# Kernel tuning notes

Hardware: AMD Instinct MI355X
Metric: run time of the kernel (lower is better)

Reference implementation:

```python
import jax, jax.numpy as jnp
import numpy as np

NEG_BIG = -9e15
ALPHA = 0.2  # leaky relu slope


def setup_inputs() -> dict:
    key = jax.random.key(0)
    k1, k2, k3, k4 = jax.random.split(key, 4)
    B, N, Fin, Fout = 8, 2048, 128, 64
    h = jax.random.normal(k1, (B, N, Fin), dtype=jnp.float32)
    adj = jax.random.randint(k2, (B, N, N), 0, 2, dtype=jnp.int32)
    # xavier_uniform-like init scale
    W = jax.random.uniform(k3, (Fin, Fout), dtype=jnp.float32, minval=-1.0, maxval=1.0) * (1.414 * np.sqrt(6.0 / (Fin + Fout)))
    a = jax.random.uniform(k4, (2 * Fout, 1), dtype=jnp.float32, minval=-1.0, maxval=1.0) * (1.414 * np.sqrt(6.0 / (2 * Fout + 1)))
    return {"h": h, "adj": adj, "W": W, "a": a}


def reference(h, adj, W, a):
    # h: [B,N,Fin], adj: [B,N,N], W: [Fin,Fout], a: [2*Fout,1]
    Fout = W.shape[1]
    Wh = jnp.einsum('bni,io->bno', h, W)            # [B,N,Fout]
    # e_ij = leakyrelu(a[:Fout] . Wh_i + a[Fout:] . Wh_j)  (decomposed, same math
    # as the original concat + matmul with a)
    f_src = Wh @ a[:Fout, 0]                        # [B,N]
    f_dst = Wh @ a[Fout:, 0]                        # [B,N]
    e = f_src[:, :, None] + f_dst[:, None, :]       # [B,N,N]
    e = jnp.where(e > 0, e, ALPHA * e)              # leaky relu
    e = jnp.where(adj > 0, e, NEG_BIG)              # mask
    attention = jax.nn.softmax(e, axis=2)           # [B,N,N]
    h_prime = jnp.einsum('bnm,bmo->bno', attention, Wh)
    return jax.nn.elu(h_prime)
```

## Files before the change

### kernel.cpp

```cpp
#include <hip/hip_runtime.h>
#include <hip/hip_bf16.h>

constexpr int Bb  = 8;
constexpr int Nn  = 2048;
constexpr int FIN = 128;
constexpr int FOUT = 64;
constexpr float LOG2E = 1.4426950408889634f;

typedef __bf16 bf16x8 __attribute__((ext_vector_type(8)));
typedef __bf16 bf16x2 __attribute__((ext_vector_type(2)));
typedef float  f32x4  __attribute__((ext_vector_type(4)));
typedef int    i32x4  __attribute__((ext_vector_type(4)));
typedef unsigned int u32;

__device__ __forceinline__ u32 f2bf_bits(float f) {
    u32 u = __builtin_bit_cast(u32, f);
    return (u + 0x7FFFu + ((u >> 16) & 1u)) >> 16;
}

__global__ __launch_bounds__(256) void gat_k1(
        const float* __restrict__ h, const float* __restrict__ W,
        const float* __restrict__ a, __bf16* __restrict__ whfrag,
        float* __restrict__ fs, float* __restrict__ fd) {
    const int blk = blockIdx.x;
    const int b   = blk >> 6;
    const int t32 = blk & 63;
    const int n0  = t32 * 32;
    const int l   = threadIdx.x & 63;
    const int w   = __builtin_amdgcn_readfirstlane((int)(threadIdx.x >> 6));

    __shared__ __align__(16) float hT[32][FIN];

    {
        const float4* hb = reinterpret_cast<const float4*>(h + (size_t)(b * Nn + n0) * FIN);
        float4* dst = reinterpret_cast<float4*>(&hT[0][0]);
#pragma unroll
        for (int k = 0; k < 4; ++k) {
            const int flat = threadIdx.x + k * 256;
            dst[flat] = hb[flat];
        }
    }
    __syncthreads();

    const float a0 = a[l];
    const float a1 = a[FOUT + l];

    float acc[8];
#pragma unroll
    for (int r = 0; r < 8; ++r) acc[r] = 0.f;

#pragma unroll 1
    for (int c0 = 0; c0 < FIN; c0 += 32) {
        float wreg[32];
#pragma unroll
        for (int cc = 0; cc < 32; ++cc) wreg[cc] = W[(c0 + cc) * FOUT + l];
#pragma unroll
        for (int r = 0; r < 8; ++r) {
            const int row = w * 8 + r;
#pragma unroll
            for (int cc = 0; cc < 32; ++cc)
                acc[r] = fmaf(hT[row][c0 + cc], wreg[cc], acc[r]);
        }
    }

#pragma unroll
    for (int r = 0; r < 8; ++r) {
        float s0 = acc[r] * a0;
        float s1 = acc[r] * a1;
#pragma unroll
        for (int off = 32; off >= 1; off >>= 1) {
            s0 += __shfl_xor(s0, off, 64);
            s1 += __shfl_xor(s1, off, 64);
        }
        if (l == 0) {
            fs[b * Nn + n0 + w * 8 + r] = s0 * LOG2E;
            fd[b * Nn + n0 + w * 8 + r] = s1 * LOG2E;
        }
    }

    u32 pk[4];
#pragma unroll
    for (int i = 0; i < 4; ++i)
        pk[i] = f2bf_bits(acc[2 * i]) | (f2bf_bits(acc[2 * i + 1]) << 16);
    const int slotg = ((b * 64 + t32) * 4 + (l >> 4)) * 64 + ((w << 4) | (l & 15));
    reinterpret_cast<uint4*>(whfrag)[slotg] = make_uint4(pk[0], pk[1], pk[2], pk[3]);
}

__global__ __launch_bounds__(256, 3) void gat_k2(
        const int* __restrict__ adj, const __bf16* __restrict__ whfrag,
        const float* __restrict__ fs, const float* __restrict__ fd,
        float* __restrict__ out) {
    const int blk = blockIdx.x;
    const int b   = blk >> 7;
    const int i0  = (blk & 127) * 16;
    const int l   = threadIdx.x & 63;
    const int w   = __builtin_amdgcn_readfirstlane((int)(threadIdx.x >> 6));

    __shared__ __align__(16) char  aLDS[4 * 8192];
    __shared__ f32x4 comb[4][4][64];
    __shared__ float zpart[4][16];

    const int hi = l >> 5;
    const int lo = l & 31;
    const int g  = l >> 4;
    const int jc = l & 15;

    char* myA = aLDS + w * 8192;

    float fs_loc[8];
#pragma unroll
    for (int t = 0; t < 8; ++t) fs_loc[t] = fs[b * Nn + i0 + 2 * t + hi];

    const int    jq0  = w * 512;
    const float* fdp  = fd + b * Nn + jq0 + lo * 4;
    const int*   adj0 = adj + (size_t)(b * Nn + i0 + hi) * Nn + jq0 + lo * 4;

    const bf16x8* bfr = reinterpret_cast<const bf16x8*>(whfrag)
                        + (size_t)(b * 256) * 64 + l;

    f32x4 acc[4] = {{0,0,0,0},{0,0,0,0},{0,0,0,0},{0,0,0,0}};
    f32x4 accz   = {0.f, 0.f, 0.f, 0.f};

    bf16x8 onesv;
#pragma unroll
    for (int i = 0; i < 8; ++i) onesv[i] = (__bf16)1.0f;

    i32x4 adjT[2][8];
    f32x4 fdQ[2];

#pragma unroll
    for (int t = 0; t < 8; ++t)
        adjT[0][t] = *reinterpret_cast<const i32x4*>(adj0 + (size_t)(2 * t) * Nn);
    fdQ[0] = *reinterpret_cast<const f32x4*>(fdp);

#pragma unroll 2
    for (int it = 0; it < 4; ++it) {
        const int cur = it & 1, nxt = cur ^ 1;
        if (it < 3) {
#pragma unroll
            for (int t = 0; t < 8; ++t)
                adjT[nxt][t] = *reinterpret_cast<const i32x4*>(
                                   adj0 + (size_t)(2 * t) * Nn + (it + 1) * 128);
            fdQ[nxt] = *reinterpret_cast<const f32x4*>(fdp + (it + 1) * 128);
        }

        char* buf = myA + cur * 4096;
#pragma unroll
        for (int t = 0; t < 8; ++t) {
            const int row = 2 * t + hi;
            float pv[4];
#pragma unroll
            for (int q = 0; q < 4; ++q) {
                float e  = fs_loc[t] + fdQ[cur][q];
                float lr = fmaxf(e, 0.2f * e);
                float p  = exp2f(lr);
                pv[q] = (adjT[cur][t][q] > 0) ? p : 0.f;
            }
            u32 w0 = __builtin_bit_cast(u32, (bf16x2){(__bf16)pv[0], (__bf16)pv[1]});
            u32 w1 = __builtin_bit_cast(u32, (bf16x2){(__bf16)pv[2], (__bf16)pv[3]});
            const int boff = (row * 256 + lo * 8) ^ ((row & 7) << 4);
            *reinterpret_cast<uint2*>(buf + boff) = make_uint2(w0, w1);
        }

        asm volatile("s_waitcnt lgkmcnt(0)" ::: "memory");
        __builtin_amdgcn_sched_barrier(0x20);

#pragma unroll
        for (int kb = 0; kb < 4; ++kb) {
            const int rbyte = (((l & 15) * 256 + kb * 64 + (l >> 4) * 16)
                               ^ ((l & 7) << 4));
            bf16x8 av = *reinterpret_cast<const bf16x8*>(buf + rbyte);
            const int t32 = w * 16 + it * 4 + kb;
#pragma unroll
            for (int o16 = 0; o16 < 4; ++o16)
                acc[o16] = __builtin_amdgcn_mfma_f32_16x16x32_bf16(
                               av, bfr[(t32 * 4 + o16) * 64], acc[o16], 0, 0, 0);
            accz = __builtin_amdgcn_mfma_f32_16x16x32_bf16(av, onesv, accz, 0, 0, 0);
        }
    }

    if ((l & 15) == 0) {
#pragma unroll
        for (int r = 0; r < 4; ++r) zpart[w][(l >> 4) * 4 + r] = accz[r];
    }
#pragma unroll
    for (int o16 = 0; o16 < 4; ++o16) comb[w][o16][l] = acc[o16];
    __syncthreads();

    f32x4 res = comb[0][w][l];
#pragma unroll
    for (int wp = 1; wp < 4; ++wp) res += comb[wp][w][l];

#pragma unroll
    for (int r = 0; r < 4; ++r) {
        const int row = g * 4 + r;
        float z = zpart[0][row] + zpart[1][row] + zpart[2][row] + zpart[3][row];
        float v = res[r] / z;
        v = v > 0.f ? v : expm1f(v);
        out[(size_t)(b * Nn + i0 + row) * FOUT + w * 16 + jc] = v;
    }
}

extern "C" void kernel_launch(void* const* d_in, const int* in_sizes, int n_in,
                              void* d_out, int out_size, void* d_ws, size_t ws_size,
                              hipStream_t stream) {
    const float* h   = (const float*)d_in[0];
    const int*   adj = (const int*)d_in[1];
    const float* W   = (const float*)d_in[2];
    const float* a   = (const float*)d_in[3];
    float* out = (float*)d_out;

    __bf16* whfrag = (__bf16*)d_ws;
    float*  fs     = (float*)((char*)d_ws + (size_t)Bb * Nn * FOUT * 2);
    float*  fd     = fs + Bb * Nn;

    gat_k1<<<dim3(Bb * 64), dim3(256), 0, stream>>>(h, W, a, whfrag, fs, fd);
    gat_k2<<<dim3(Bb * 128), dim3(256), 0, stream>>>(adj, whfrag, fs, fd, out);
}
```

Before: 55.59 us.

## Restructure GAT attention loop into 64-column steps with triple-buffered prefetch

The per-wave attention loop now processes 64 columns per step instead of 128, with each lane handling four consecutive rows. Adjacency and f_dst loads are prefetched two steps ahead through a three-slot register ring, in a fully unrolled macro. Per-wave LDS shrinks to half and launch bounds rise to 4 blocks per CU, aiming for more occupancy and deeper latency hiding on the adjacency stream. The trade-off is more LDS wait/sync points per column and possible register pressure under the tighter occupancy bound.

```diff
diff --git a/kernel.cpp b/kernel.cpp
--- a/kernel.cpp
+++ b/kernel.cpp
@@ -86,7 +86,7 @@
     reinterpret_cast<uint4*>(whfrag)[slotg] = make_uint4(pk[0], pk[1], pk[2], pk[3]);
 }
 
-__global__ __launch_bounds__(256, 3) void gat_k2(
+__global__ __launch_bounds__(256, 4) void gat_k2(
         const int* __restrict__ adj, const __bf16* __restrict__ whfrag,
         const float* __restrict__ fs, const float* __restrict__ fd,
         float* __restrict__ out) {
@@ -96,27 +96,25 @@
     const int l   = threadIdx.x & 63;
     const int w   = __builtin_amdgcn_readfirstlane((int)(threadIdx.x >> 6));
 
-    __shared__ __align__(16) char  aLDS[4 * 8192];
+    __shared__ __align__(16) char  aLDS[4 * 4096];
     __shared__ f32x4 comb[4][4][64];
     __shared__ float zpart[4][16];
 
-    const int hi = l >> 5;
-    const int lo = l & 31;
     const int g  = l >> 4;
     const int jc = l & 15;
 
-    char* myA = aLDS + w * 8192;
-
-    float fs_loc[8];
-#pragma unroll
-    for (int t = 0; t < 8; ++t) fs_loc[t] = fs[b * Nn + i0 + 2 * t + hi];
+    char* myA = aLDS + w * 4096;
+
+    float fs_loc[4];
+#pragma unroll
+    for (int rr = 0; rr < 4; ++rr) fs_loc[rr] = fs[b * Nn + i0 + g * 4 + rr];
 
     const int    jq0  = w * 512;
-    const float* fdp  = fd + b * Nn + jq0 + lo * 4;
-    const int*   adj0 = adj + (size_t)(b * Nn + i0 + hi) * Nn + jq0 + lo * 4;
+    const float* fdp  = fd + b * Nn + jq0 + jc * 4;
+    const int*   adj0 = adj + (size_t)(b * Nn + i0 + g * 4) * Nn + jq0 + jc * 4;
 
     const bf16x8* bfr = reinterpret_cast<const bf16x8*>(whfrag)
-                        + (size_t)(b * 256) * 64 + l;
+                        + (size_t)((b * 64 + w * 16) * 4) * 64 + l;
 
     f32x4 acc[4] = {{0,0,0,0},{0,0,0,0},{0,0,0,0},{0,0,0,0}};
     f32x4 accz   = {0.f, 0.f, 0.f, 0.f};
@@ -125,59 +123,79 @@
 #pragma unroll
     for (int i = 0; i < 8; ++i) onesv[i] = (__bf16)1.0f;
 
-    i32x4 adjT[2][8];
-    f32x4 fdQ[2];
-
-#pragma unroll
-    for (int t = 0; t < 8; ++t)
-        adjT[0][t] = *reinterpret_cast<const i32x4*>(adj0 + (size_t)(2 * t) * Nn);
-    fdQ[0] = *reinterpret_cast<const f32x4*>(fdp);
-
-#pragma unroll 2
-    for (int it = 0; it < 4; ++it) {
-        const int cur = it & 1, nxt = cur ^ 1;
-        if (it < 3) {
-#pragma unroll
-            for (int t = 0; t < 8; ++t)
-                adjT[nxt][t] = *reinterpret_cast<const i32x4*>(
-                                   adj0 + (size_t)(2 * t) * Nn + (it + 1) * 128);
-            fdQ[nxt] = *reinterpret_cast<const f32x4*>(fdp + (it + 1) * 128);
-        }
-
-        char* buf = myA + cur * 4096;
-#pragma unroll
-        for (int t = 0; t < 8; ++t) {
-            const int row = 2 * t + hi;
-            float pv[4];
-#pragma unroll
-            for (int q = 0; q < 4; ++q) {
-                float e  = fs_loc[t] + fdQ[cur][q];
-                float lr = fmaxf(e, 0.2f * e);
-                float p  = exp2f(lr);
-                pv[q] = (adjT[cur][t][q] > 0) ? p : 0.f;
-            }
-            u32 w0 = __builtin_bit_cast(u32, (bf16x2){(__bf16)pv[0], (__bf16)pv[1]});
-            u32 w1 = __builtin_bit_cast(u32, (bf16x2){(__bf16)pv[2], (__bf16)pv[3]});
-            const int boff = (row * 256 + lo * 8) ^ ((row & 7) << 4);
-            *reinterpret_cast<uint2*>(buf + boff) = make_uint2(w0, w1);
-        }
-
-        asm volatile("s_waitcnt lgkmcnt(0)" ::: "memory");
-        __builtin_amdgcn_sched_barrier(0x20);
-
-#pragma unroll
-        for (int kb = 0; kb < 4; ++kb) {
-            const int rbyte = (((l & 15) * 256 + kb * 64 + (l >> 4) * 16)
-                               ^ ((l & 7) << 4));
-            bf16x8 av = *reinterpret_cast<const bf16x8*>(buf + rbyte);
-            const int t32 = w * 16 + it * 4 + kb;
-#pragma unroll
-            for (int o16 = 0; o16 < 4; ++o16)
-                acc[o16] = __builtin_amdgcn_mfma_f32_16x16x32_bf16(
-                               av, bfr[(t32 * 4 + o16) * 64], acc[o16], 0, 0, 0);
-            accz = __builtin_amdgcn_mfma_f32_16x16x32_bf16(av, onesv, accz, 0, 0, 0);
-        }
-    }
+    i32x4 adjR[3][4];
+    f32x4 fdR[3];
+
+#pragma unroll
+    for (int rr = 0; rr < 4; ++rr) {
+        adjR[0][rr] = *reinterpret_cast<const i32x4*>(adj0 + (size_t)rr * Nn);
+        adjR[1][rr] = *reinterpret_cast<const i32x4*>(adj0 + (size_t)rr * Nn + 64);
+    }
+    fdR[0] = *reinterpret_cast<const f32x4*>(fdp);
+    fdR[1] = *reinterpret_cast<const f32x4*>(fdp + 64);
+
+#define GAT_STEP(IT, CUR, PRE)                                                 \
+  {                                                                            \
+    if ((IT) + 2 < 8) {                \
+      _Pragma("unroll")                                                        \
+      for (int rr = 0; rr < 4; ++rr)                                           \
+        adjR[PRE][rr] = *reinterpret_cast<const i32x4*>(                       \
+            adj0 + (size_t)rr * Nn + ((IT) + 2) * 64);                         \
+      fdR[PRE] = *reinterpret_cast<const f32x4*>(fdp + ((IT) + 2) * 64);       \
+    }                                                                          \
+    char* buf = myA + ((IT) & 1) * 2048;                                       \
+    _Pragma("unroll")                                                          \
+    for (int rr = 0; rr < 4; ++rr) {                                           \
+      const int row = g * 4 + rr;                                              \
+      u32 wds[2];                                                              \
+      _Pragma("unroll")                                                        \
+      for (int hp = 0; hp < 2; ++hp) {                                         \
+        float pv[2];                                                           \
+        _Pragma("unroll")                                                      \
+        for (int q = 0; q < 2; ++q) {                                          \
+          const int jj = hp * 2 + q;                                           \
+          float e  = fs_loc[rr] + fdR[CUR][jj];                                \
+          float lr = fmaxf(e, 0.2f * e);          \
+          float p  = exp2f(lr);                 \
+          pv[q] = (adjR[CUR][rr][jj] > 0) ? p : 0.f;                           \
+        }                                                                      \
+        wds[hp] = __builtin_bit_cast(u32,                                      \
+                      (bf16x2){(__bf16)pv[0], (__bf16)pv[1]});                 \
+      }                                                                        \
+      const int boff = (row * 128 + jc * 8) ^ ((row & 7) << 4);                \
+      *reinterpret_cast<uint2*>(buf + boff) = make_uint2(wds[0], wds[1]);      \
+    }                                                                          \
+    asm volatile("s_waitcnt lgkmcnt(0)" ::: "memory");                         \
+    __builtin_amdgcn_sched_barrier(0x20);            \
+    {                                                                          \
+      const int rb0 = (((l & 15) * 128 + g * 16) ^ ((l & 7) << 4));            \
+      bf16x8 av = *reinterpret_cast<const bf16x8*>(buf + rb0);                 \
+      _Pragma("unroll")                                                        \
+      for (int o16 = 0; o16 < 4; ++o16)                                        \
+        acc[o16] = __builtin_amdgcn_mfma_f32_16x16x32_bf16(                    \
+            av, bfr[(((IT) * 2 + 0) * 4 + o16) * 64], acc[o16], 0, 0, 0);      \
+      accz = __builtin_amdgcn_mfma_f32_16x16x32_bf16(av, onesv, accz, 0, 0, 0);\
+    }                                                                          \
+    {                                                                          \
+      const int rb1 = (((l & 15) * 128 + 64 + g * 16) ^ ((l & 7) << 4));       \
+      bf16x8 av = *reinterpret_cast<const bf16x8*>(buf + rb1);                 \
+      _Pragma("unroll")                                                        \
+      for (int o16 = 0; o16 < 4; ++o16)                                        \
+        acc[o16] = __builtin_amdgcn_mfma_f32_16x16x32_bf16(                    \
+            av, bfr[(((IT) * 2 + 1) * 4 + o16) * 64], acc[o16], 0, 0, 0);      \
+      accz = __builtin_amdgcn_mfma_f32_16x16x32_bf16(av, onesv, accz, 0, 0, 0);\
+    }                                                                          \
+  }
+
+    GAT_STEP(0, 0, 2)
+    GAT_STEP(1, 1, 0)
+    GAT_STEP(2, 2, 1)
+    GAT_STEP(3, 0, 2)
+    GAT_STEP(4, 1, 0)
+    GAT_STEP(5, 2, 1)
+    GAT_STEP(6, 0, 2)
+    GAT_STEP(7, 1, 0)
+#undef GAT_STEP
 
     if ((l & 15) == 0) {
 #pragma unroll
```

Measured after the change: 47.58 us. 14.4% less time.

## Precompress adjacency into bitmask and build attention MFMA operands in registers

Applied to the files above, without the earlier changes.

The first kernel gains extra blocks that read the int32 adjacency matrix and pack it into a 1-bit-per-entry mask, running alongside the Wh projection blocks. The attention kernel then reads the small mask instead of the full adjacency matrix. It builds the bf16 probability fragments directly in registers in MFMA layout, which removes the LDS staging round-trip and its waits. Total adjacency traffic is unchanged but moves into a streaming pack kernel, and the mask adds an extra workspace write and read.

```diff
diff --git a/kernel.cpp b/kernel.cpp
--- a/kernel.cpp
+++ b/kernel.cpp
@@ -12,24 +12,51 @@
 typedef float  f32x4  __attribute__((ext_vector_type(4)));
 typedef int    i32x4  __attribute__((ext_vector_type(4)));
 typedef unsigned int u32;
+typedef unsigned long long u64;
 
 __device__ __forceinline__ u32 f2bf_bits(float f) {
     u32 u = __builtin_bit_cast(u32, f);
     return (u + 0x7FFFu + ((u >> 16) & 1u)) >> 16;
 }
 
-__global__ __launch_bounds__(256) void gat_k1(
-        const float* __restrict__ h, const float* __restrict__ W,
-        const float* __restrict__ a, __bf16* __restrict__ whfrag,
-        float* __restrict__ fs, float* __restrict__ fd) {
+__global__ __launch_bounds__(256) void gat_k01(
+        const float* __restrict__ h, const int* __restrict__ adj,
+        const float* __restrict__ W, const float* __restrict__ a,
+        __bf16* __restrict__ whfrag, float* __restrict__ fs,
+        float* __restrict__ fd, u64* __restrict__ mask) {
+    __shared__ __align__(16) float hT[32][FIN];
+
+    const int l = threadIdx.x & 63;
+    const int w = __builtin_amdgcn_readfirstlane((int)(threadIdx.x >> 6));
+
+    if (blockIdx.x >= 512) {
+        const size_t gw = (size_t)(blockIdx.x - 512) * 4 + w;
+        const int* p  = adj + gw * 4096 + 4 * l;
+        u64* mout     = mask + gw * 64;
+        i32x4 vv[2];
+        vv[0] = *reinterpret_cast<const i32x4*>(p);
+#pragma unroll
+        for (int i = 0; i < 16; ++i) {
+            const int cur = i & 1;
+            if (i < 15)
+                vv[cur ^ 1] = *reinterpret_cast<const i32x4*>(p + (i + 1) * 256);
+            const i32x4 v = vv[cur];
+            u32 nib = (v[0] > 0 ? 1u : 0u) | (v[1] > 0 ? 2u : 0u) |
+                      (v[2] > 0 ? 4u : 0u) | (v[3] > 0 ? 8u : 0u);
+            u32 x = nib | (((u32)__shfl_xor((int)nib, 1)) << 4);
+            x |= ((u32)__shfl_xor((int)x, 2)) << 8;
+            x |= ((u32)__shfl_xor((int)x, 4)) << 16;
+            u32 hi = (u32)__shfl_xor((int)x, 8);
+            if ((l & 15) == 0)
+                mout[i * 4 + (l >> 4)] = (u64)x | ((u64)hi << 32);
+        }
+        return;
+    }
+
     const int blk = blockIdx.x;
     const int b   = blk >> 6;
     const int t32 = blk & 63;
     const int n0  = t32 * 32;
-    const int l   = threadIdx.x & 63;
-    const int w   = __builtin_amdgcn_readfirstlane((int)(threadIdx.x >> 6));
-
-    __shared__ __align__(16) float hT[32][FIN];
 
     {
         const float4* hb = reinterpret_cast<const float4*>(h + (size_t)(b * Nn + n0) * FIN);
@@ -86,8 +113,8 @@
     reinterpret_cast<uint4*>(whfrag)[slotg] = make_uint4(pk[0], pk[1], pk[2], pk[3]);
 }
 
-__global__ __launch_bounds__(256, 3) void gat_k2(
-        const int* __restrict__ adj, const __bf16* __restrict__ whfrag,
+__global__ __launch_bounds__(256, 4) void gat_k2(
+        const u64* __restrict__ mask, const __bf16* __restrict__ whfrag,
         const float* __restrict__ fs, const float* __restrict__ fd,
         float* __restrict__ out) {
     const int blk = blockIdx.x;
@@ -96,27 +123,19 @@
     const int l   = threadIdx.x & 63;
     const int w   = __builtin_amdgcn_readfirstlane((int)(threadIdx.x >> 6));
 
-    __shared__ __align__(16) char  aLDS[4 * 8192];
     __shared__ f32x4 comb[4][4][64];
     __shared__ float zpart[4][16];
 
-    const int hi = l >> 5;
-    const int lo = l & 31;
-    const int g  = l >> 4;
-    const int jc = l & 15;
-
-    char* myA = aLDS + w * 8192;
-
-    float fs_loc[8];
-#pragma unroll
-    for (int t = 0; t < 8; ++t) fs_loc[t] = fs[b * Nn + i0 + 2 * t + hi];
-
-    const int    jq0  = w * 512;
-    const float* fdp  = fd + b * Nn + jq0 + lo * 4;
-    const int*   adj0 = adj + (size_t)(b * Nn + i0 + hi) * Nn + jq0 + lo * 4;
+    const int row16 = l & 15;
+    const int seg8  = (l >> 4) * 8;
+
+    const float fsr = fs[b * Nn + i0 + row16];
+
+    const u64*   mrow = mask + ((size_t)b * Nn + i0 + row16) * 32 + w * 8;
+    const float* fdq  = fd + b * Nn + w * 512 + seg8;
 
     const bf16x8* bfr = reinterpret_cast<const bf16x8*>(whfrag)
-                        + (size_t)(b * 256) * 64 + l;
+                        + (size_t)((b * 64 + w * 16) * 4) * 64 + l;
 
     f32x4 acc[4] = {{0,0,0,0},{0,0,0,0},{0,0,0,0},{0,0,0,0}};
     f32x4 accz   = {0.f, 0.f, 0.f, 0.f};
@@ -125,56 +144,42 @@
 #pragma unroll
     for (int i = 0; i < 8; ++i) onesv[i] = (__bf16)1.0f;
 
-    i32x4 adjT[2][8];
-    f32x4 fdQ[2];
-
-#pragma unroll
-    for (int t = 0; t < 8; ++t)
-        adjT[0][t] = *reinterpret_cast<const i32x4*>(adj0 + (size_t)(2 * t) * Nn);
-    fdQ[0] = *reinterpret_cast<const f32x4*>(fdp);
-
 #pragma unroll 2
-    for (int it = 0; it < 4; ++it) {
-        const int cur = it & 1, nxt = cur ^ 1;
-        if (it < 3) {
-#pragma unroll
-            for (int t = 0; t < 8; ++t)
-                adjT[nxt][t] = *reinterpret_cast<const i32x4*>(
-                                   adj0 + (size_t)(2 * t) * Nn + (it + 1) * 128);
-            fdQ[nxt] = *reinterpret_cast<const f32x4*>(fdp + (it + 1) * 128);
-        }
-
-        char* buf = myA + cur * 4096;
-#pragma unroll
-        for (int t = 0; t < 8; ++t) {
-            const int row = 2 * t + hi;
-            float pv[4];
-#pragma unroll
-            for (int q = 0; q < 4; ++q) {
-                float e  = fs_loc[t] + fdQ[cur][q];
+    for (int jt = 0; jt < 8; ++jt) {
+        const u64 mk = mrow[jt];
+#pragma unroll
+        for (int kb = 0; kb < 2; ++kb) {
+            const f32x4 fd0 = *reinterpret_cast<const f32x4*>(fdq + jt * 64 + kb * 32);
+            const f32x4 fd1 = *reinterpret_cast<const f32x4*>(fdq + jt * 64 + kb * 32 + 4);
+            const u32 mb = (u32)(mk >> (kb * 32 + seg8)) & 0xffu;
+
+            float pv[8];
+#pragma unroll
+            for (int r = 0; r < 4; ++r) {
+                float e  = fsr + fd0[r];
                 float lr = fmaxf(e, 0.2f * e);
                 float p  = exp2f(lr);
-                pv[q] = (adjT[cur][t][q] > 0) ? p : 0.f;
+                pv[r] = ((mb >> r) & 1u) ? p : 0.f;
             }
-            u32 w0 = __builtin_bit_cast(u32, (bf16x2){(__bf16)pv[0], (__bf16)pv[1]});
-            u32 w1 = __builtin_bit_cast(u32, (bf16x2){(__bf16)pv[2], (__bf16)pv[3]});
-            const int boff = (row * 256 + lo * 8) ^ ((row & 7) << 4);
-            *reinterpret_cast<uint2*>(buf + boff) = make_uint2(w0, w1);
-        }
-
-        asm volatile("s_waitcnt lgkmcnt(0)" ::: "memory");
-        __builtin_amdgcn_sched_barrier(0x20);
-
-#pragma unroll
-        for (int kb = 0; kb < 4; ++kb) {
-            const int rbyte = (((l & 15) * 256 + kb * 64 + (l >> 4) * 16)
-                               ^ ((l & 7) << 4));
-            bf16x8 av = *reinterpret_cast<const bf16x8*>(buf + rbyte);
-            const int t32 = w * 16 + it * 4 + kb;
+#pragma unroll
+            for (int r = 0; r < 4; ++r) {
+                float e  = fsr + fd1[r];
+                float lr = fmaxf(e, 0.2f * e);
+                float p  = exp2f(lr);
+                pv[4 + r] = ((mb >> (4 + r)) & 1u) ? p : 0.f;
+            }
+
+            uint4 pk4;
+            pk4.x = __builtin_bit_cast(u32, (bf16x2){(__bf16)pv[0], (__bf16)pv[1]});
+            pk4.y = __builtin_bit_cast(u32, (bf16x2){(__bf16)pv[2], (__bf16)pv[3]});
+            pk4.z = __builtin_bit_cast(u32, (bf16x2){(__bf16)pv[4], (__bf16)pv[5]});
+            pk4.w = __builtin_bit_cast(u32, (bf16x2){(__bf16)pv[6], (__bf16)pv[7]});
+            const bf16x8 av = __builtin_bit_cast(bf16x8, pk4);
+
 #pragma unroll
             for (int o16 = 0; o16 < 4; ++o16)
                 acc[o16] = __builtin_amdgcn_mfma_f32_16x16x32_bf16(
-                               av, bfr[(t32 * 4 + o16) * 64], acc[o16], 0, 0, 0);
+                               av, bfr[((jt * 2 + kb) * 4 + o16) * 64], acc[o16], 0, 0, 0);
             accz = __builtin_amdgcn_mfma_f32_16x16x32_bf16(av, onesv, accz, 0, 0, 0);
         }
     }
@@ -193,11 +198,11 @@
 
 #pragma unroll
     for (int r = 0; r < 4; ++r) {
-        const int row = g * 4 + r;
+        const int row = (l >> 4) * 4 + r;
         float z = zpart[0][row] + zpart[1][row] + zpart[2][row] + zpart[3][row];
         float v = res[r] / z;
         v = v > 0.f ? v : expm1f(v);
-        out[(size_t)(b * Nn + i0 + row) * FOUT + w * 16 + jc] = v;
+        out[(size_t)(b * Nn + i0 + row) * FOUT + w * 16 + (l & 15)] = v;
     }
 }
 
@@ -213,7 +218,8 @@
     __bf16* whfrag = (__bf16*)d_ws;
     float*  fs     = (float*)((char*)d_ws + (size_t)Bb * Nn * FOUT * 2);
     float*  fd     = fs + Bb * Nn;
-
-    gat_k1<<<dim3(Bb * 64), dim3(256), 0, stream>>>(h, W, a, whfrag, fs, fd);
-    gat_k2<<<dim3(Bb * 128), dim3(256), 0, stream>>>(adj, whfrag, fs, fd, out);
-}
+    u64*    mask   = (u64*)((char*)d_ws + (4u << 20));
+
+    gat_k01<<<dim3(512 + 2048), dim3(256), 0, stream>>>(h, adj, W, a, whfrag, fs, fd, mask);
+    gat_k2 <<<dim3(Bb * 128),   dim3(256), 0, stream>>>(mask, whfrag, fs, fd, out);
+}
```

New measurement: 60.40 us. 1.09x slower.
